# Kernel optimization log

Hardware: AMD Instinct MI355X
Metric: run time of the kernel (lower is better)

Reference implementation:

```python
import jax, jax.numpy as jnp
import numpy as np

EMB_DIM = 768
QKV_DIM = 64
NUM_HEAD = 12


def setup_inputs() -> dict:
    key = jax.random.key(0)
    k1, k2, k3 = jax.random.split(key, 3)
    z = jax.random.normal(k1, (16, 1024, EMB_DIM), dtype=jnp.float32)
    U_qkv = jax.random.normal(k2, (NUM_HEAD, 3, EMB_DIM, QKV_DIM), dtype=jnp.float32) * (1.0 / np.sqrt(EMB_DIM))
    U_msa = jax.random.normal(k3, (NUM_HEAD * QKV_DIM, EMB_DIM), dtype=jnp.float32) * (1.0 / np.sqrt(NUM_HEAD * QKV_DIM))
    return {"z": z, "U_qkv": U_qkv, "U_msa": U_msa}


def reference(z, U_qkv, U_msa):
    # z: [b, n, e]; U_qkv: [h, 3, e, d]; U_msa: [h*d, e]
    qkv = jnp.einsum("bne,hked->khbnd", z, U_qkv)  # [3, h, b, n, d]
    q, k, v = qkv[0], qkv[1], qkv[2]               # each [h, b, n, d]
    scale = 1.0 / jnp.sqrt(jnp.asarray(q.shape[-1], dtype=z.dtype))
    logits = jnp.einsum("hbnd,hbmd->hbnm", q, k) * scale  # [h, b, n, n]
    attn = jax.nn.softmax(logits, axis=-1)
    o = jnp.einsum("hbnm,hbmd->bnhd", attn, v)     # [b, n, h, d]
    b, n = o.shape[0], o.shape[1]
    o = o.reshape(b, n, -1)                        # [b, n, h*d]
    return o @ U_msa                               # [b, n, e]
```

## Files before the change

### kernel.cpp

```cpp
#include <hip/hip_runtime.h>
#include <hip/hip_bf16.h>

typedef _Float16 f16x8 __attribute__((ext_vector_type(8)));
typedef _Float16 f16x4 __attribute__((ext_vector_type(4)));
typedef float f32x4 __attribute__((ext_vector_type(4)));

#define MFMA32(a, b, c) __builtin_amdgcn_mfma_f32_16x16x32_f16(a, b, c, 0, 0, 0)
#define MFMA16(a, b, c) __builtin_amdgcn_mfma_f32_16x16x16f16(a, b, c, 0, 0, 0)

#define GLOAD_LDS16(g, l)                                         \
  __builtin_amdgcn_global_load_lds(                               \
      (const __attribute__((address_space(1))) void*)(g),         \
      (__attribute__((address_space(3))) void*)(l), 16, 0, 0)

__global__ __launch_bounds__(256) void tconv_kernel(
    const float* __restrict__ in, _Float16* __restrict__ out, int R, int C) {
  size_t bat = (size_t)blockIdx.y * R * C;
  int o = blockIdx.x * 256 + threadIdx.x;
  if (o < R * C) {
    int c = o / R, r = o - c * R;
    out[bat + o] = (_Float16)in[bat + (size_t)r * C + c];
  }
}

__global__ __launch_bounds__(256) void cvt16_kernel(
    const float* __restrict__ in, _Float16* __restrict__ out, int n) {
  int i = (blockIdx.x * 256 + threadIdx.x) * 8;
  if (i < n) {
    float4 a = *(const float4*)(in + i);
    float4 b = *(const float4*)(in + i + 4);
    f16x8 cv;
    cv[0] = (_Float16)a.x; cv[1] = (_Float16)a.y;
    cv[2] = (_Float16)a.z; cv[3] = (_Float16)a.w;
    cv[4] = (_Float16)b.x; cv[5] = (_Float16)b.y;
    cv[6] = (_Float16)b.z; cv[7] = (_Float16)b.w;
    *(f16x8*)(out + i) = cv;
  }
}

__global__ __launch_bounds__(512) void qkv_gemm_kernel(
    const _Float16* __restrict__ zh, const _Float16* __restrict__ Ut,
    _Float16* __restrict__ Qf, _Float16* __restrict__ Kf,
    _Float16* __restrict__ Vt) {
  __shared__ _Float16 As[2][256 * 64];
  __shared__ _Float16 Bs[2][256 * 64];

  const int tid = threadIdx.x;
  const int wid = tid >> 6, lane = tid & 63, quad = lane >> 4, l16 = lane & 15;
  const int wr = wid >> 2, wc = wid & 3;

  const int m0 = blockIdx.x * 256;
  const int by = blockIdx.y;
  const int n0 = by * 256;

  const int srow = lane >> 3;
  const int scol = ((lane & 7) ^ srow) << 3;
  const _Float16* Ag = zh + (size_t)(m0 + srow) * 768 + scol;
  const _Float16* Bg = Ut + (size_t)(n0 + srow) * 768 + scol;

#define STAGE_A(buf, t)                                                  \
  {                                                                      \
    _Pragma("unroll") for (int hf = 0; hf < 2; ++hf)                     \
        _Pragma("unroll") for (int i = 0; i < 2; ++i) {                  \
      const int rb = hf * 128 + (wid * 2 + i) * 8;                       \
      GLOAD_LDS16(Ag + (size_t)rb * 768 + (t) * 64,                      \
                  (char*)&As[buf][0] + rb * 128);                        \
    }                                                                    \
  }
#define STAGE_B(buf, t)                                                  \
  {                                                                      \
    _Pragma("unroll") for (int hf = 0; hf < 2; ++hf)                     \
        _Pragma("unroll") for (int i = 0; i < 2; ++i) {                  \
      const int rb = hf * 128 + (wid * 2 + i) * 8;                       \
      GLOAD_LDS16(Bg + (size_t)rb * 768 + (t) * 64,                      \
                  (char*)&Bs[buf][0] + rb * 128);                        \
    }                                                                    \
  }

  f32x4 acc[8][4] = {};

  STAGE_A(0, 0);
  STAGE_B(0, 0);

  for (int t = 0; t < 12; ++t) {
    const int cur = t & 1;
    asm volatile("s_waitcnt vmcnt(0)" ::: "memory");
    asm volatile("s_barrier" ::: "memory");
#pragma unroll
    for (int q = 0; q < 4; ++q) {
      const int mh = q >> 1, nh = q & 1;
      f16x8 af[4][2], bf[2][2];
#pragma unroll
      for (int mf = 0; mf < 4; ++mf) {
        const int r = wr * 128 + mh * 64 + mf * 16 + l16;
#pragma unroll
        for (int ks = 0; ks < 2; ++ks)
          af[mf][ks] =
              *(const f16x8*)((const char*)&As[cur][0] + r * 128 +
                              ((ks * 64 + quad * 16) ^ ((r & 7) << 4)));
      }
#pragma unroll
      for (int j = 0; j < 2; ++j) {
        const int r = wc * 64 + nh * 32 + j * 16 + l16;
#pragma unroll
        for (int ks = 0; ks < 2; ++ks)
          bf[j][ks] =
              *(const f16x8*)((const char*)&Bs[cur][0] + r * 128 +
                              ((ks * 64 + quad * 16) ^ ((r & 7) << 4)));
      }
      if (t < 11) {
        if (q == 0) STAGE_A(cur ^ 1, t + 1)
        else if (q == 1) STAGE_B(cur ^ 1, t + 1)
      }
      asm volatile("s_barrier" ::: "memory");
      __builtin_amdgcn_s_setprio(1);
#pragma unroll
      for (int mf = 0; mf < 4; ++mf)
#pragma unroll
        for (int j = 0; j < 2; ++j)
#pragma unroll
          for (int ks = 0; ks < 2; ++ks)
            acc[mh * 4 + mf][nh * 2 + j] =
                MFMA32(af[mf][ks], bf[j][ks], acc[mh * 4 + mf][nh * 2 + j]);
      __builtin_amdgcn_s_setprio(0);
      asm volatile("s_barrier" ::: "memory");
    }
  }

  const int g = by * 4 + wc;
  const int hd = g / 3, kk = g - hd * 3;
#pragma unroll
  for (int mfp = 0; mfp < 8; ++mfp) {
#pragma unroll
    for (int nfp = 0; nfp < 4; ++nfp) {
      const int dd = nfp * 16 + l16;
#pragma unroll
      for (int r = 0; r < 4; ++r) {
        int m = m0 + wr * 128 + mfp * 16 + quad * 4 + r;
        int b = m >> 10, n = m & 1023;
        _Float16 val = (_Float16)acc[mfp][nfp][r];
        if (kk == 0)
          Qf[(((size_t)hd * 16 + b) * 1024 + n) * 64 + dd] = val;
        else if (kk == 1)
          Kf[(((size_t)hd * 16 + b) * 1024 + n) * 64 + dd] = val;
        else
          Vt[(((size_t)hd * 16 + b) * 64 + dd) * 1024 + n] = val;
      }
    }
  }
#undef STAGE_A
#undef STAGE_B
}

__global__ __launch_bounds__(256) void attn_kernel(
    const _Float16* __restrict__ Qf, const _Float16* __restrict__ Kf,
    const _Float16* __restrict__ Vt, _Float16* __restrict__ Of) {
  __shared__ _Float16 Ks[2][64][72];
  __shared__ _Float16 Vs[2][64][72];

  const int tid = threadIdx.x;
  const int wv = tid >> 6, lane = tid & 63, quad = lane >> 4, l16 = lane & 15;

  const int flat = blockIdx.x;
  const int swz = (flat & 7) * 192 + (flat >> 3);
  const int hb = swz >> 3;
  const int h = hb >> 4, b = hb & 15;
  const _Float16* Q = Qf + (size_t)hb * 65536;
  const _Float16* K = Kf + (size_t)hb * 65536;
  const _Float16* V = Vt + (size_t)hb * 65536;
  const int q0 = (swz & 7) * 128 + wv * 32;

  const _Float16 cs = (_Float16)0.18033688011112042f;
  f16x8 qfr[2][2];
#pragma unroll
  for (int mi = 0; mi < 2; ++mi) {
    const _Float16* qp = Q + (size_t)(q0 + mi * 16 + l16) * 64 + quad * 8;
    qfr[mi][0] = *(const f16x8*)qp * cs;
    qfr[mi][1] = *(const f16x8*)(qp + 32) * cs;
  }

  const int r0 = tid >> 3, c0 = (tid & 7) << 3;
  const _Float16* Kst = K + (size_t)r0 * 64 + c0;
  const _Float16* Vst = V + (size_t)r0 * 1024 + c0;

  uint4 kreg[2], vreg[2];
#pragma unroll
  for (int i = 0; i < 2; ++i) {
    kreg[i] = *(const uint4*)(Kst + i * 2048);
    vreg[i] = *(const uint4*)(Vst + i * 32768);
  }
#pragma unroll
  for (int i = 0; i < 2; ++i) {
    *(uint4*)&Ks[0][r0 + i * 32][c0] = kreg[i];
    *(uint4*)&Vs[0][r0 + i * 32][c0] = vreg[i];
  }
  __syncthreads();

  f32x4 o[2][4] = {};
  float lsum[2] = {};

  for (int t = 0; t < 16; ++t) {
    const int cur = t & 1;
    if (t < 15) {
      int n1 = (t + 1) * 64;
#pragma unroll
      for (int i = 0; i < 2; ++i) {
        kreg[i] = *(const uint4*)(Kst + (size_t)n1 * 64 + i * 2048);
        vreg[i] = *(const uint4*)(Vst + n1 + i * 32768);
      }
    }

    f32x4 st[2][4] = {};
    __builtin_amdgcn_s_setprio(1);
#pragma unroll
    for (int ct = 0; ct < 4; ++ct) {
      f16x8 kf0 = *(const f16x8*)&Ks[cur][ct * 16 + l16][quad * 8];
      f16x8 kf1 = *(const f16x8*)&Ks[cur][ct * 16 + l16][32 + quad * 8];
#pragma unroll
      for (int mi = 0; mi < 2; ++mi) {
        st[mi][ct] = MFMA32(kf0, qfr[mi][0], st[mi][ct]);
        st[mi][ct] = MFMA32(kf1, qfr[mi][1], st[mi][ct]);
      }
    }
    __builtin_amdgcn_s_setprio(0);

    f16x4 pa[2][4];
#pragma unroll
    for (int mi = 0; mi < 2; ++mi)
#pragma unroll
      for (int ct = 0; ct < 4; ++ct)
#pragma unroll
        for (int r = 0; r < 4; ++r) {
          float p = __builtin_amdgcn_exp2f(st[mi][ct][r]);
          lsum[mi] += p;
          pa[mi][ct][r] = (_Float16)p;
        }

    __builtin_amdgcn_s_setprio(1);
#pragma unroll
    for (int dt = 0; dt < 4; ++dt) {
#pragma unroll
      for (int kb = 0; kb < 4; ++kb) {
        f16x4 vf = *(const f16x4*)&Vs[cur][dt * 16 + l16][kb * 16 + quad * 4];
#pragma unroll
        for (int mi = 0; mi < 2; ++mi)
          o[mi][dt] = MFMA16(pa[mi][kb], vf, o[mi][dt]);
      }
    }
    __builtin_amdgcn_s_setprio(0);

    if (t < 15) {
#pragma unroll
      for (int i = 0; i < 2; ++i) {
        *(uint4*)&Ks[cur ^ 1][r0 + i * 32][c0] = kreg[i];
        *(uint4*)&Vs[cur ^ 1][r0 + i * 32][c0] = vreg[i];
      }
      __syncthreads();
    }
  }

#pragma unroll
  for (int mi = 0; mi < 2; ++mi) {
    float s = lsum[mi];
    s += __shfl_xor(s, 16, 64);
    s += __shfl_xor(s, 32, 64);
    lsum[mi] = s;
  }

#pragma unroll
  for (int mi = 0; mi < 2; ++mi) {
#pragma unroll
    for (int r = 0; r < 4; ++r) {
      float inv = 1.f / __shfl(lsum[mi], quad * 4 + r, 64);
      int n = q0 + mi * 16 + quad * 4 + r;
#pragma unroll
      for (int dt = 0; dt < 4; ++dt) {
        int dd = dt * 16 + l16;
        __builtin_nontemporal_store(
            (_Float16)(o[mi][dt][r] * inv),
            &Of[((size_t)b * 1024 + n) * 768 + h * 64 + dd]);
      }
    }
  }
}

__global__ __launch_bounds__(256) void out_gemm_kernel(
    const _Float16* __restrict__ A, const _Float16* __restrict__ Bt,
    float* __restrict__ Cout) {
  __shared__ _Float16 As[2][128 * 64];
  __shared__ _Float16 Bs[2][128 * 64];

  const int tid = threadIdx.x;
  const int wv = tid >> 6, lane = tid & 63, quad = lane >> 4, l16 = lane & 15;

  const int m0 = blockIdx.x * 128;
  const int n0 = blockIdx.y * 128;

  const int srow = lane >> 3;
  const int scol = ((lane & 7) ^ srow) << 3;
  const _Float16* Ag = A + (size_t)(m0 + srow) * 768 + scol;
  const _Float16* Bg = Bt + (size_t)(n0 + srow) * 768 + scol;

  const int cbq = quad * 16;

  f32x4 acc[2][8] = {};

#pragma unroll
  for (int i = 0; i < 4; ++i) {
    const int rb = (i * 4 + wv) * 8;
    GLOAD_LDS16(Ag + (size_t)rb * 768, (char*)As[0] + rb * 128);
    GLOAD_LDS16(Bg + (size_t)rb * 768, (char*)Bs[0] + rb * 128);
  }
  asm volatile("s_waitcnt vmcnt(0)" ::: "memory");
  __builtin_amdgcn_s_barrier();

  for (int t = 0; t < 12; ++t) {
    const int cur = t & 1;
    if (t < 11) {
      const int k1 = (t + 1) * 64;
#pragma unroll
      for (int i = 0; i < 4; ++i) {
        const int rb = (i * 4 + wv) * 8;
        GLOAD_LDS16(Ag + (size_t)rb * 768 + k1,
                    (char*)As[cur ^ 1] + rb * 128);
        GLOAD_LDS16(Bg + (size_t)rb * 768 + k1,
                    (char*)Bs[cur ^ 1] + rb * 128);
      }
    }
#pragma unroll
    for (int ks = 0; ks < 2; ++ks) {
      f16x8 af[2], bfr[8];
#pragma unroll
      for (int rt = 0; rt < 2; ++rt) {
        const int r = wv * 32 + rt * 16 + l16;
        af[rt] = *(const f16x8*)((const char*)As[cur] + r * 128 +
                                 ((ks * 64 + cbq) ^ ((r & 7) << 4)));
      }
#pragma unroll
      for (int ct = 0; ct < 8; ++ct) {
        const int r = ct * 16 + l16;
        bfr[ct] = *(const f16x8*)((const char*)Bs[cur] + r * 128 +
                                  ((ks * 64 + cbq) ^ ((r & 7) << 4)));
      }
#pragma unroll
      for (int rt = 0; rt < 2; ++rt)
#pragma unroll
        for (int ct = 0; ct < 8; ++ct)
          acc[rt][ct] = MFMA32(af[rt], bfr[ct], acc[rt][ct]);
    }
    if (t < 11) {
      asm volatile("s_waitcnt vmcnt(0)" ::: "memory");
      __builtin_amdgcn_s_barrier();
    }
  }

#pragma unroll
  for (int rt = 0; rt < 2; ++rt) {
#pragma unroll
    for (int ct = 0; ct < 8; ++ct) {
#pragma unroll
      for (int r = 0; r < 4; ++r) {
        int m = m0 + wv * 32 + rt * 16 + quad * 4 + r;
        int n = n0 + ct * 16 + l16;
        __builtin_nontemporal_store(acc[rt][ct][r],
                                    &Cout[(size_t)m * 768 + n]);
      }
    }
  }
}

extern "C" void kernel_launch(void* const* d_in, const int* in_sizes, int n_in,
                              void* d_out, int out_size, void* d_ws,
                              size_t ws_size, hipStream_t stream) {
  const float* z = (const float*)d_in[0];
  const float* Uqkv = (const float*)d_in[1];
  const float* Umsa = (const float*)d_in[2];

  char* ws = (char*)d_ws;
  _Float16* Ut_qkv = (_Float16*)(ws);
  _Float16* Ut_msa = (_Float16*)(ws + 3538944);
  _Float16* zh = (_Float16*)(ws + 4718592);
  _Float16* Of = zh;
  _Float16* Qf = (_Float16*)(ws + 29884416);
  _Float16* Kf = (_Float16*)(ws + 55050240);
  _Float16* Vt = (_Float16*)(ws + 80216064);

  tconv_kernel<<<dim3(192, 36), 256, 0, stream>>>(Uqkv, Ut_qkv, 768, 64);
  tconv_kernel<<<dim3(2304, 1), 256, 0, stream>>>(Umsa, Ut_msa, 768, 768);
  cvt16_kernel<<<dim3(6144, 1), 256, 0, stream>>>(z, zh, 16384 * 768);

  qkv_gemm_kernel<<<dim3(64, 9), 512, 0, stream>>>(zh, Ut_qkv, Qf, Kf, Vt);
  attn_kernel<<<dim3(1536, 1), 256, 0, stream>>>(Qf, Kf, Vt, Of);
  out_gemm_kernel<<<dim3(128, 6), 256, 0, stream>>>(Of, Ut_msa,
                                                    (float*)d_out);
}
```

Before: 355.9 us.

## Split QKV GEMM K-tile into half-tiles with finer-grained vmcnt pipelining

```diff
diff --git a/kernel.cpp b/kernel.cpp
--- a/kernel.cpp
+++ b/kernel.cpp
@@ -42,88 +42,86 @@
     const _Float16* __restrict__ zh, const _Float16* __restrict__ Ut,
     _Float16* __restrict__ Qf, _Float16* __restrict__ Kf,
     _Float16* __restrict__ Vt) {
-  __shared__ _Float16 As[2][256 * 64];
-  __shared__ _Float16 Bs[2][256 * 64];
+  __shared__ _Float16 S[65536];
 
   const int tid = threadIdx.x;
-  const int wid = tid >> 6, lane = tid & 63, quad = lane >> 4, l16 = lane & 15;
+  const int wid = tid >> 6, lane = tid & 63;
+  const int quad = lane >> 4, l16 = lane & 15;
   const int wr = wid >> 2, wc = wid & 3;
 
   const int m0 = blockIdx.x * 256;
   const int by = blockIdx.y;
   const int n0 = by * 256;
 
-  const int srow = lane >> 3;
-  const int scol = ((lane & 7) ^ srow) << 3;
-  const _Float16* Ag = zh + (size_t)(m0 + srow) * 768 + scol;
-  const _Float16* Bg = Ut + (size_t)(n0 + srow) * 768 + scol;
-
-#define STAGE_A(buf, t)                                                  \
-  {                                                                      \
-    _Pragma("unroll") for (int hf = 0; hf < 2; ++hf)                     \
-        _Pragma("unroll") for (int i = 0; i < 2; ++i) {                  \
-      const int rb = hf * 128 + (wid * 2 + i) * 8;                       \
-      GLOAD_LDS16(Ag + (size_t)rb * 768 + (t) * 64,                      \
-                  (char*)&As[buf][0] + rb * 128);                        \
-    }                                                                    \
-  }
-#define STAGE_B(buf, t)                                                  \
-  {                                                                      \
-    _Pragma("unroll") for (int hf = 0; hf < 2; ++hf)                     \
-        _Pragma("unroll") for (int i = 0; i < 2; ++i) {                  \
-      const int rb = hf * 128 + (wid * 2 + i) * 8;                       \
-      GLOAD_LDS16(Bg + (size_t)rb * 768 + (t) * 64,                      \
-                  (char*)&Bs[buf][0] + rb * 128);                        \
-    }                                                                    \
-  }
+  const int srow = lane >> 2;
+  const int scol = ((lane & 3) ^ ((lane >> 3) & 3)) * 8;
+  const _Float16* Agb = zh + (size_t)(m0 + srow) * 768 + scol;
+  const _Float16* Bgb = Ut + (size_t)(n0 + srow) * 768 + scol;
+
+  const int slotb = (quad ^ ((l16 >> 1) & 3)) * 16;
+
+#define QKV_STAGE(mat, ks, buf, t)                                        \
+  {                                                                       \
+    const _Float16* gsrc = (mat) ? Bgb : Agb;                             \
+    _Pragma("unroll") for (int j = 0; j < 2; ++j) {                       \
+      GLOAD_LDS16(gsrc + (size_t)((wid * 2 + j) * 16) * 768 +             \
+                      (t) * 64 + (ks) * 32,                               \
+                  (char*)S + (buf) * 65536 + (mat) * 32768 +              \
+                      (ks) * 16384 + (wid * 2 + j) * 1024);               \
+    }                                                                     \
+  }
+
+#define QKV_PHASE(ks, mh, STAGE_STMT, WAIT_STMT)                          \
+  {                                                                       \
+    const char* Abase = (const char*)S + cur * 65536 + (ks) * 16384;      \
+    const char* Bbase = Abase + 32768;                                    \
+    f16x8 af[4], bf[2][2];                                                \
+    _Pragma("unroll") for (int mf = 0; mf < 4; ++mf) {                    \
+      const int r = wr * 128 + (mh) * 64 + mf * 16 + l16;                 \
+      af[mf] = *(const f16x8*)(Abase + r * 64 + slotb);                   \
+    }                                                                     \
+    _Pragma("unroll") for (int nh = 0; nh < 2; ++nh)                      \
+        _Pragma("unroll") for (int j = 0; j < 2; ++j) {                   \
+      const int r = wc * 64 + nh * 32 + j * 16 + l16;                     \
+      bf[nh][j] = *(const f16x8*)(Bbase + r * 64 + slotb);                \
+    }                                                                     \
+    STAGE_STMT;                                                           \
+    asm volatile("s_barrier" ::: "memory");                               \
+    __builtin_amdgcn_s_setprio(1);                                        \
+    _Pragma("unroll") for (int mf = 0; mf < 4; ++mf)                      \
+        _Pragma("unroll") for (int nh = 0; nh < 2; ++nh)                  \
+            _Pragma("unroll") for (int j = 0; j < 2; ++j)                 \
+                acc[(mh)*4 + mf][nh * 2 + j] = MFMA32(                    \
+                    af[mf], bf[nh][j], acc[(mh)*4 + mf][nh * 2 + j]);     \
+    __builtin_amdgcn_s_setprio(0);                                        \
+    WAIT_STMT;                                                            \
+    asm volatile("s_barrier" ::: "memory");                               \
+  }
+
+#define VMC4 asm volatile("s_waitcnt vmcnt(4)" ::: "memory")
+#define VMC0 asm volatile("s_waitcnt vmcnt(0)" ::: "memory")
 
   f32x4 acc[8][4] = {};
 
-  STAGE_A(0, 0);
-  STAGE_B(0, 0);
+  QKV_STAGE(0, 0, 0, 0);
+  QKV_STAGE(1, 0, 0, 0);
+  QKV_STAGE(0, 1, 0, 0);
+  QKV_STAGE(1, 1, 0, 0);
+  VMC4;
+  asm volatile("s_barrier" ::: "memory");
 
   for (int t = 0; t < 12; ++t) {
-    const int cur = t & 1;
-    asm volatile("s_waitcnt vmcnt(0)" ::: "memory");
-    asm volatile("s_barrier" ::: "memory");
-#pragma unroll
-    for (int q = 0; q < 4; ++q) {
-      const int mh = q >> 1, nh = q & 1;
-      f16x8 af[4][2], bf[2][2];
-#pragma unroll
-      for (int mf = 0; mf < 4; ++mf) {
-        const int r = wr * 128 + mh * 64 + mf * 16 + l16;
-#pragma unroll
-        for (int ks = 0; ks < 2; ++ks)
-          af[mf][ks] =
-              *(const f16x8*)((const char*)&As[cur][0] + r * 128 +
-                              ((ks * 64 + quad * 16) ^ ((r & 7) << 4)));
-      }
-#pragma unroll
-      for (int j = 0; j < 2; ++j) {
-        const int r = wc * 64 + nh * 32 + j * 16 + l16;
-#pragma unroll
-        for (int ks = 0; ks < 2; ++ks)
-          bf[j][ks] =
-              *(const f16x8*)((const char*)&Bs[cur][0] + r * 128 +
-                              ((ks * 64 + quad * 16) ^ ((r & 7) << 4)));
-      }
-      if (t < 11) {
-        if (q == 0) STAGE_A(cur ^ 1, t + 1)
-        else if (q == 1) STAGE_B(cur ^ 1, t + 1)
-      }
-      asm volatile("s_barrier" ::: "memory");
-      __builtin_amdgcn_s_setprio(1);
-#pragma unroll
-      for (int mf = 0; mf < 4; ++mf)
-#pragma unroll
-        for (int j = 0; j < 2; ++j)
-#pragma unroll
-          for (int ks = 0; ks < 2; ++ks)
-            acc[mh * 4 + mf][nh * 2 + j] =
-                MFMA32(af[mf][ks], bf[j][ks], acc[mh * 4 + mf][nh * 2 + j]);
-      __builtin_amdgcn_s_setprio(0);
-      asm volatile("s_barrier" ::: "memory");
+    const int cur = t & 1, nb = cur ^ 1;
+    if (t < 11) {
+      QKV_PHASE(0, 0, QKV_STAGE(0, 0, nb, t + 1), );
+      QKV_PHASE(0, 1, QKV_STAGE(1, 0, nb, t + 1), VMC4);
+      QKV_PHASE(1, 0, QKV_STAGE(0, 1, nb, t + 1), );
+      QKV_PHASE(1, 1, QKV_STAGE(1, 1, nb, t + 1), VMC4);
+    } else {
+      QKV_PHASE(0, 0, , );
+      QKV_PHASE(0, 1, , VMC0);
+      QKV_PHASE(1, 0, , );
+      QKV_PHASE(1, 1, , );
     }
   }
 
@@ -148,8 +146,10 @@
       }
     }
   }
-#undef STAGE_A
-#undef STAGE_B
+#undef QKV_STAGE
+#undef QKV_PHASE
+#undef VMC4
+#undef VMC0
 }
 
 __global__ __launch_bounds__(256) void attn_kernel(
```

After: 360.0 us. No clear change (+1.2%).
